# Optimization experiments

Measured on AMD Instinct MI355X. Metric: run time of the kernel, lower is better.

The kernel has to match this reference:

```python
import jax, jax.numpy as jnp
import numpy as np

N_NODES = 4096
N_EDGES = 16384
F_IN = 64
F_EDGE = 16
HID = 128
OUT = 64
N_GRAPHS = 32


def _encoder(x, edge_index, edge_attr, batch, p):
    N = x.shape[0]
    src, dst = edge_index[0], edge_index[1]
    # EdgeMLP: [E, F_edge] -> [E, F_in * HID] per-edge weight matrices
    h = jax.nn.relu(edge_attr @ p['e_w1'] + p['e_b1'])
    h = jax.nn.relu(h @ p['e_w2'] + p['e_b2'])
    Wmat = (h @ p['e_w3'] + p['e_b3']).reshape(-1, x.shape[1], p['root_w'].shape[1])  # [E, F_in, HID]
    # NNConv: message = x_src @ W_edge, scatter-add to dst, plus root transform + bias
    msg = jnp.einsum('ei,eio->eo', x[src], Wmat)  # [E, HID]
    agg = jax.ops.segment_sum(msg, dst, num_segments=N)
    h1 = jax.nn.relu(agg + x @ p['root_w'] + p['conv1_b'])  # [N, HID]
    # GATConv (1 head, concat=False) with self-loops (PyG default)
    loop = jnp.arange(N, dtype=src.dtype)
    si = jnp.concatenate([src, loop])
    di = jnp.concatenate([dst, loop])
    hp = h1 @ p['gat_w']  # [N, HID]
    a_s = hp @ p['att_src']  # [N]
    a_d = hp @ p['att_dst']  # [N]
    e = jax.nn.leaky_relu(a_s[si] + a_d[di], negative_slope=0.2)
    m = jax.ops.segment_max(e, di, num_segments=N)
    ex = jnp.exp(e - m[di])
    denom = jax.ops.segment_sum(ex, di, num_segments=N)
    alpha = ex / (denom[di] + 1e-16)
    h2 = jax.ops.segment_sum(alpha[:, None] * hp[si], di, num_segments=N) + p['gat_b']
    h2 = jax.nn.relu(h2)
    # global mean pool over graphs
    s = jax.ops.segment_sum(h2, batch, num_segments=N_GRAPHS)
    cnt = jax.ops.segment_sum(jnp.ones((N,), h2.dtype), batch, num_segments=N_GRAPHS)
    pooled = s / jnp.maximum(cnt, 1.0)[:, None]
    return jax.nn.relu(pooled @ p['fc1_w'] + p['fc1_b'])  # [B, OUT]


def setup_inputs() -> dict:
    key = jax.random.key(0)
    ks = jax.random.split(key, 24)
    d = {}
    d['x1'] = jax.random.normal(ks[0], (N_NODES, F_IN), jnp.float32)
    d['edge_index1'] = jax.random.randint(ks[1], (2, N_EDGES), 0, N_NODES)
    d['edge_attr1'] = jax.random.normal(ks[2], (N_EDGES, F_EDGE), jnp.float32)
    d['batch1'] = jnp.sort(jax.random.randint(ks[3], (N_NODES,), 0, N_GRAPHS))
    d['x2'] = jax.random.normal(ks[4], (N_NODES, F_IN), jnp.float32)
    d['edge_index2'] = jax.random.randint(ks[5], (2, N_EDGES), 0, N_NODES)
    d['edge_attr2'] = jax.random.normal(ks[6], (N_EDGES, F_EDGE), jnp.float32)
    d['batch2'] = jnp.sort(jax.random.randint(ks[7], (N_NODES,), 0, N_GRAPHS))

    def lin(k, fi, fo):
        return jax.random.normal(k, (fi, fo), jnp.float32) * (fi ** -0.5)

    d['e_w1'] = lin(ks[8], F_EDGE, 128); d['e_b1'] = jnp.zeros((128,), jnp.float32)
    d['e_w2'] = lin(ks[9], 128, 64); d['e_b2'] = jnp.zeros((64,), jnp.float32)
    d['e_w3'] = lin(ks[10], 64, F_IN * HID); d['e_b3'] = jnp.zeros((F_IN * HID,), jnp.float32)
    d['root_w'] = lin(ks[11], F_IN, HID); d['conv1_b'] = jnp.zeros((HID,), jnp.float32)
    d['gat_w'] = lin(ks[12], HID, HID)
    d['att_src'] = jax.random.normal(ks[13], (HID,), jnp.float32) * (HID ** -0.5)
    d['att_dst'] = jax.random.normal(ks[14], (HID,), jnp.float32) * (HID ** -0.5)
    d['gat_b'] = jnp.zeros((HID,), jnp.float32)
    d['fc1_w'] = lin(ks[15], HID, OUT); d['fc1_b'] = jnp.zeros((OUT,), jnp.float32)
    d['fc2_w'] = lin(ks[16], OUT, 1); d['fc2_b'] = jnp.zeros((1,), jnp.float32)
    return d


def reference(x1, edge_index1, edge_attr1, batch1, x2, edge_index2, edge_attr2, batch2,
              e_w1, e_b1, e_w2, e_b2, e_w3, e_b3, root_w, conv1_b,
              gat_w, att_src, att_dst, gat_b, fc1_w, fc1_b, fc2_w, fc2_b):
    p = dict(e_w1=e_w1, e_b1=e_b1, e_w2=e_w2, e_b2=e_b2, e_w3=e_w3, e_b3=e_b3,
             root_w=root_w, conv1_b=conv1_b, gat_w=gat_w, att_src=att_src,
             att_dst=att_dst, gat_b=gat_b, fc1_w=fc1_w, fc1_b=fc1_b,
             fc2_w=fc2_w, fc2_b=fc2_b)
    z1 = _encoder(x1, edge_index1, edge_attr1, batch1, p)
    z2 = _encoder(x2, edge_index2, edge_attr2, batch2, p)
    z = jnp.abs(z1 - z2) @ fc2_w + fc2_b  # [B, 1]
    return jax.nn.sigmoid(z).squeeze(1)  # [B]
```

## Files before the change

### kernel.cpp

```cpp
#include <hip/hip_runtime.h>
#include <hip/hip_bf16.h>
#include <math.h>

#define NN 4096
#define NE 16384
#define FIN 64
#define FE 16
#define HIDD 128
#define OUTD 64
#define NG 32
#define EP (NE + NN)
#define KSPLIT 2
#define NCH (64 / KSPLIT)

typedef __attribute__((ext_vector_type(4))) unsigned u4v;
typedef __attribute__((ext_vector_type(4))) float f4v;
typedef _Float16 f16x8 __attribute__((ext_vector_type(8)));

union FragH { u4v u; f16x8 h; };
union FH2 { _Float16 f[2]; unsigned u; };
union F16x8U { _Float16 f[8]; u4v u; };

#define PB_EMLP  4096
#define PB_BIAS  (PB_EMLP + 4096)
#define PB_HIST  (PB_BIAS + 32)
#define PB_TOTAL (PB_HIST + 64)

__global__ void k_prep(const float* __restrict__ ea0, const float* __restrict__ ea1,
                       const float* __restrict__ w1, const float* __restrict__ b1,
                       const float* __restrict__ w2, const float* __restrict__ b2,
                       const float* __restrict__ w3,
                       const float* __restrict__ X0, const float* __restrict__ X1,
                       const float* __restrict__ b3,
                       const int* __restrict__ ei0, const int* __restrict__ ei1,
                       unsigned short* __restrict__ B1t,
                       float* __restrict__ h0, float* __restrict__ h1g,
                       float* __restrict__ Bb0, float* __restrict__ Bb1,
                       int* __restrict__ rowcnt) {
    int b = blockIdx.x, t = threadIdx.x;
    if (b < PB_EMLP) {
        int gi = b >> 11;
        int e0 = (b & 2047) * 8;
        const float* ea = gi ? ea1 : ea0;
        float* hout = gi ? h1g : h0;
        __shared__ float h1s[8][HIDD];
#pragma unroll
        for (int r = 0; r < 4; ++r) {
            int idx = r * 256 + t;
            int e1 = idx >> 7, j = idx & 127;
            float acc = b1[j];
#pragma unroll
            for (int i = 0; i < FE; ++i) acc += ea[(e0 + e1) * FE + i] * w1[i * HIDD + j];
            h1s[e1][j] = fmaxf(acc, 0.f);
        }
        __syncthreads();
#pragma unroll
        for (int r = 0; r < 2; ++r) {
            int idx = r * 256 + t;
            int e1 = idx >> 6, j = idx & 63;
            float acc = b2[j];
#pragma unroll 16
            for (int k = 0; k < HIDD; ++k) acc += h1s[e1][k] * w2[k * 64 + j];
            hout[(size_t)(e0 + e1) * 64 + j] = fmaxf(acc, 0.f);
        }
    } else if (b < PB_BIAS) {
        int bb = b - PB_EMLP;
        int gi = bb >> 11;
        int n = (bb & 2047) * 2 + (t >> 7);
        int o = t & 127;
        const float* X = gi ? X1 : X0;
        float* Bb = gi ? Bb1 : Bb0;
        float acc = 0.f;
#pragma unroll 16
        for (int i = 0; i < FIN; ++i) acc += X[n * FIN + i] * b3[i * HIDD + o];
        Bb[(size_t)n * HIDD + o] = acc;
    } else if (b < PB_HIST) {
        int tid = (b - PB_BIAS) * 256 + t;
        for (int idx = tid; idx < 2 * EP; idx += 32 * 256) {
            int gi = idx / EP, e = idx % EP;
            const int* dst = (gi ? ei1 : ei0) + NE;
            int d = (e < NE) ? dst[e] : e - NE;
            atomicAdd(&rowcnt[gi * NN + d], 1);
        }
    } else {
        __shared__ float lds[64 * 129];
        int c = b - PB_HIST;
#pragma unroll
        for (int r = 0; r < 32; ++r) {
            int idx = r * 256 + t;
            lds[(idx >> 7) * 129 + (idx & 127)] = w3[(size_t)c * 8192 + idx];
        }
        __syncthreads();
#pragma unroll
        for (int r = 0; r < 32; ++r) {
            int e = r * 256 + t;
            float v = lds[(e & 63) * 129 + (e >> 6)];
            union { _Float16 f; unsigned short u; } cv;
            cv.f = (_Float16)v;
            B1t[(size_t)c * 8192 + e] = cv.u;
        }
    }
}

__global__ void k_scan(const int* __restrict__ rowcnt, int* __restrict__ rowptr,
                       const int* __restrict__ batch0, const int* __restrict__ batch1,
                       int* __restrict__ br) {
    int b = blockIdx.x;
    if (b < 2) {
        int gi = b;
        const int* cnt = rowcnt + gi * NN;
        int* rp = rowptr + gi * (NN + 1);
        int t = threadIdx.x;
        int lane = t & 63, w = t >> 6;
        int base = t * 4;
        int v0 = cnt[base], v1 = cnt[base + 1], v2 = cnt[base + 2], v3 = cnt[base + 3];
        int s = v0 + v1 + v2 + v3;
        int inc = s;
#pragma unroll
        for (int off = 1; off < 64; off <<= 1) {
            int u = __shfl_up(inc, off);
            if (lane >= off) inc += u;
        }
        __shared__ int wsum[16];
        if (lane == 63) wsum[w] = inc;
        __syncthreads();
        if (t < 16) {
            int ws = wsum[t];
            int wi = ws;
#pragma unroll
            for (int off = 1; off < 16; off <<= 1) {
                int u = __shfl_up(wi, off);
                if (t >= off) wi += u;
            }
            wsum[t] = wi - ws;
        }
        __syncthreads();
        int run = wsum[w] + inc - s;
        rp[base] = run; run += v0;
        rp[base + 1] = run; run += v1;
        rp[base + 2] = run; run += v2;
        rp[base + 3] = run; run += v3;
        if (t == 1023) rp[NN] = run;
    } else {
        int t = threadIdx.x;
        if (t < 66) {
            int gi = t / 33, g = t % 33;
            const int* batch = gi ? batch1 : batch0;
            int lo = 0, hi = NN;
            while (lo < hi) {
                int mid = (lo + hi) >> 1;
                if (batch[mid] < g) lo = mid + 1; else hi = mid;
            }
            br[gi * 33 + g] = lo;
        }
    }
}

__global__ void k_fill(const int* __restrict__ ei0, const int* __restrict__ ei1,
                       const int* __restrict__ rowptr, int* __restrict__ cnt2,
                       int* __restrict__ adj) {
    int idx = blockIdx.x * 256 + threadIdx.x;
    if (idx >= 2 * EP) return;
    int gi = idx / EP, e = idx % EP;
    const int* dst = (gi ? ei1 : ei0) + NE;
    int d = (e < NE) ? dst[e] : e - NE;
    int pos = rowptr[gi * (NN + 1) + d] + atomicAdd(&cnt2[gi * NN + d], 1);
    adj[gi * EP + pos] = e;
}

__global__ void __launch_bounds__(128, 2)
k_nnconv(const float* __restrict__ x0, const float* __restrict__ x1,
         const float* __restrict__ h_0, const float* __restrict__ h_1,
         const unsigned short* __restrict__ B1t,
         const float* __restrict__ Bb0, const float* __restrict__ Bb1,
         const int* __restrict__ ei0, const int* __restrict__ ei1,
         _Float16* __restrict__ msgh) {
    __shared__ __align__(16) float sm[32 * 128];
    int gi = blockIdx.z;
    const float* x = gi ? x1 : x0;
    const float* hh = gi ? h_1 : h_0;
    const float* Bb = gi ? Bb1 : Bb0;
    const int* src = gi ? ei1 : ei0;

    int t = threadIdx.x;
    int e0 = blockIdx.x * 64;
    int z = blockIdx.y;
    int ch = t >> 6;
    int l = t & 63, q4 = l >> 4, c16 = l & 15;

    FragH xf[4][2];
    int hb_[4];
#pragma unroll
    for (int mf = 0; mf < 4; ++mf) {
        int s_ = src[e0 + mf * 16 + c16];
        hb_[mf] = (e0 + mf * 16 + c16) * 64 + z * NCH;
        const float* xr = &x[(size_t)s_ * FIN];
#pragma unroll
        for (int kf = 0; kf < 2; ++kf) {
            float xv[8];
            *(float4*)&xv[0] = *(const float4*)&xr[kf * 32 + q4 * 8];
            *(float4*)&xv[4] = *(const float4*)&xr[kf * 32 + q4 * 8 + 4];
            u4v w;
#pragma unroll
            for (int p = 0; p < 4; ++p) {
                FH2 c2;
                c2.f[0] = (_Float16)xv[2 * p];
                c2.f[1] = (_Float16)xv[2 * p + 1];
                w[p] = c2.u;
            }
            xf[mf][kf].u = w;
        }
    }

    f4v acc[4][4];
#pragma unroll
    for (int a = 0; a < 4; ++a)
#pragma unroll
        for (int b = 0; b < 4; ++b) acc[a][b] = (f4v){0.f, 0.f, 0.f, 0.f};

    const u4v* bp = (const u4v*)B1t;

#define LOADF(buf, cg)                                                          \
    {                                                                           \
        const u4v* cp = bp + (size_t)(cg) * 1024;                               \
        _Pragma("unroll") for (int kf = 0; kf < 2; ++kf)                        \
        _Pragma("unroll") for (int nf = 0; nf < 4; ++nf)                        \
            buf[kf * 4 + nf].u = cp[(ch * 64 + nf * 16 + c16) * 8 + kf * 4 + q4]; \
    }

#define DOMFMA(buf)                                                             \
    {                                                                           \
        _Pragma("unroll") for (int mf = 0; mf < 4; ++mf) {                      \
            FH2 hp2;                                                            \
            hp2.f[0] = (_Float16)hvC[mf];                                       \
            hp2.f[1] = hp2.f[0];                                                \
            unsigned hw = hp2.u;                                                \
            FragH hb; hb.u = (u4v){hw, hw, hw, hw};                             \
            _Pragma("unroll") for (int kf = 0; kf < 2; ++kf) {                  \
                FragH a1;                                                       \
                a1.h = hb.h * xf[mf][kf].h;                                     \
                _Pragma("unroll") for (int nf = 0; nf < 4; ++nf)                \
                    acc[mf][nf] = __builtin_amdgcn_mfma_f32_16x16x32_f16(       \
                        a1.h, buf[kf * 4 + nf].h, acc[mf][nf], 0, 0, 0);        \
            }                                                                   \
        }                                                                       \
    }

#define STAGE(buf, cl, DO_H, DO_L)                                              \
    {                                                                           \
        if (DO_H) {                                                             \
            _Pragma("unroll") for (int mf = 0; mf < 4; ++mf)                    \
                hvN[mf] = hh[hb_[mf] + (cl) + 1];                               \
        }                                                                       \
        DOMFMA(buf);                                                            \
        if (DO_L) LOADF(buf, z * NCH + (cl) + 3);                               \
        _Pragma("unroll") for (int mf = 0; mf < 4; ++mf) hvC[mf] = hvN[mf];     \
    }

    FragH bA[8], bB[8], bC[8];
    float hvC[4], hvN[4];
    LOADF(bA, z * NCH + 0);
    LOADF(bB, z * NCH + 1);
    LOADF(bC, z * NCH + 2);
#pragma unroll
    for (int mf = 0; mf < 4; ++mf) hvC[mf] = hh[hb_[mf]];

#pragma unroll 1
    for (int cl = 0; cl < NCH - 5; cl += 3) {
        STAGE(bA, cl, 1, 1);
        STAGE(bB, cl + 1, 1, 1);
        STAGE(bC, cl + 2, 1, 1);
    }
    STAGE(bA, NCH - 5, 1, 1);
    STAGE(bB, NCH - 4, 1, 1);
    STAGE(bC, NCH - 3, 1, 0);
    STAGE(bA, NCH - 2, 1, 0);
    STAGE(bB, NCH - 1, 0, 0);
#undef STAGE
#undef LOADF
#undef DOMFMA

    _Float16* mb = msgh + (size_t)(gi * KSPLIT + z) * NE * HIDD;
    int z0 = (z == 0);
#pragma unroll
    for (int half = 0; half < 2; ++half) {
        if (half) __syncthreads();
#pragma unroll
        for (int mf2 = 0; mf2 < 2; ++mf2) {
            int mf = half * 2 + mf2;
#pragma unroll
            for (int j = 0; j < 4; ++j) {
                int rr = mf2 * 16 + q4 * 4 + j;
#pragma unroll
                for (int nf = 0; nf < 4; ++nf)
                    sm[rr * 128 + ch * 64 + nf * 16 + c16] = acc[mf][nf][j];
            }
        }
        __syncthreads();
#pragma unroll
        for (int it = 0; it < 4; ++it) {
            int u = it * 128 + t;
            int row = u >> 4, c8 = u & 15;
            int eg = e0 + half * 32 + row;
            float v[8];
            *(float4*)&v[0] = *(float4*)&sm[row * 128 + c8 * 8];
            *(float4*)&v[4] = *(float4*)&sm[row * 128 + c8 * 8 + 4];
            if (z0) {
                int s_ = src[eg];
                const float* bbr = &Bb[(size_t)s_ * HIDD + c8 * 8];
#pragma unroll
                for (int j = 0; j < 8; ++j) v[j] += bbr[j];
            }
            F16x8U cv;
#pragma unroll
            for (int j = 0; j < 8; ++j) cv.f[j] = (_Float16)v[j];
            *(u4v*)&mb[(size_t)eg * HIDD + c8 * 8] = cv.u;
        }
    }
}

__global__ void k_h1hp(const _Float16* __restrict__ msgh,
                       const int* __restrict__ rowptr, const int* __restrict__ adj,
                       const float* __restrict__ X0, const float* __restrict__ X1,
                       const float* __restrict__ rw, const float* __restrict__ cb,
                       const float* __restrict__ gw,
                       const float* __restrict__ asw, const float* __restrict__ adw,
                       float* __restrict__ hp0, float* __restrict__ hp1,
                       float* __restrict__ a_s0, float* __restrict__ a_s1,
                       float* __restrict__ a_d0, float* __restrict__ a_d1) {
    int gi = blockIdx.y;
    const float* X = gi ? X1 : X0;
    float* hp = gi ? hp1 : hp0;
    float* a_s = gi ? a_s1 : a_s0;
    float* a_d = gi ? a_d1 : a_d0;
    const int* rp = rowptr + gi * (NN + 1);
    const int* aj = adj + gi * EP;
    const _Float16* m0 = msgh + (size_t)(gi * KSPLIT + 0) * NE * HIDD;
    const _Float16* m1 = msgh + (size_t)(gi * KSPLIT + 1) * NE * HIDD;
    int n0 = blockIdx.x * 16;
    int t = threadIdx.x;
    int o = t & 127, q = t >> 7;
    __shared__ float xsh[16][FIN];
    __shared__ float h1s[16][HIDD];
    __shared__ float s1[16][2], s2[16][2];
#pragma unroll
    for (int r = 0; r < 2; ++r) {
        int idx = r * 512 + t;
        xsh[idx >> 6][idx & 63] = X[(n0 + (idx >> 6)) * FIN + (idx & 63)];
    }
    __syncthreads();
    float accs[4];
#pragma unroll
    for (int nn = 0; nn < 4; ++nn) {
        int n = n0 + q * 4 + nn;
        float acc = cb[o];
        int lo = rp[n], hi = rp[n + 1];
        for (int p = lo; p < hi; ++p) {
            int e = aj[p];
            if (e < NE) {
                size_t eo = (size_t)e * HIDD + o;
                acc += (float)m0[eo] + (float)m1[eo];
            }
        }
        accs[nn] = acc;
    }
#pragma unroll 8
    for (int i = 0; i < FIN; ++i) {
        float w = rw[i * HIDD + o];
#pragma unroll
        for (int nn = 0; nn < 4; ++nn) accs[nn] += xsh[q * 4 + nn][i] * w;
    }
#pragma unroll
    for (int nn = 0; nn < 4; ++nn) h1s[q * 4 + nn][o] = fmaxf(accs[nn], 0.f);
    __syncthreads();
#pragma unroll
    for (int nn = 0; nn < 4; ++nn) accs[nn] = 0.f;
#pragma unroll 8
    for (int k = 0; k < HIDD; ++k) {
        float w = gw[k * HIDD + o];
#pragma unroll
        for (int nn = 0; nn < 4; ++nn) accs[nn] += h1s[q * 4 + nn][k] * w;
    }
#pragma unroll
    for (int nn = 0; nn < 4; ++nn) {
        int n = n0 + q * 4 + nn;
        hp[(size_t)n * HIDD + o] = accs[nn];
        float p1 = accs[nn] * asw[o], p2 = accs[nn] * adw[o];
#pragma unroll
        for (int off = 32; off; off >>= 1) {
            p1 += __shfl_down(p1, off);
            p2 += __shfl_down(p2, off);
        }
        if ((o & 63) == 0) { s1[q * 4 + nn][o >> 6] = p1; s2[q * 4 + nn][o >> 6] = p2; }
    }
    __syncthreads();
    if (t < 16) {
        a_s[n0 + t] = s1[t][0] + s1[t][1];
        a_d[n0 + t] = s2[t][0] + s2[t][1];
    }
}

__global__ void k_gat(const int* __restrict__ rowptr, const int* __restrict__ adj,
                      const int* __restrict__ ei0, const int* __restrict__ ei1,
                      const float* __restrict__ hp0, const float* __restrict__ hp1,
                      const float* __restrict__ as0, const float* __restrict__ as1,
                      const float* __restrict__ ad0, const float* __restrict__ ad1,
                      const float* __restrict__ gb,
                      float* __restrict__ h2_0, float* __restrict__ h2_1) {
    int gi = blockIdx.y;
    const int* src = gi ? ei1 : ei0;
    const float* hp = gi ? hp1 : hp0;
    const float* a_s = gi ? as1 : as0;
    const float* a_d = gi ? ad1 : ad0;
    float* h2 = gi ? h2_1 : h2_0;
    const int* rp = rowptr + gi * (NN + 1);
    const int* aj = adj + gi * EP;
    int w = threadIdx.x >> 6, l = threadIdx.x & 63;
    int n = blockIdx.x * 4 + w;
    int lo = rp[n], deg = rp[n + 1] - lo;
    float adn = a_d[n];
    float m = -1e30f;
    for (int base = 0; base < deg; base += 64) {
        float sc = -1e30f;
        int j = base + l;
        if (j < deg) {
            int e = aj[lo + j];
            int si = (e < NE) ? src[e] : n;
            float xsc = a_s[si] + adn;
            sc = xsc > 0.f ? xsc : 0.2f * xsc;
        }
#pragma unroll
        for (int off = 32; off; off >>= 1) sc = fmaxf(sc, __shfl_xor(sc, off));
        m = fmaxf(m, sc);
    }
    float den = 0.f;
    for (int base = 0; base < deg; base += 64) {
        float ev = 0.f;
        int j = base + l;
        if (j < deg) {
            int e = aj[lo + j];
            int si = (e < NE) ? src[e] : n;
            float xsc = a_s[si] + adn;
            float sc = xsc > 0.f ? xsc : 0.2f * xsc;
            ev = expf(sc - m);
        }
#pragma unroll
        for (int off = 32; off; off >>= 1) ev += __shfl_xor(ev, off);
        den += ev;
    }
    float inv = 1.f / (den + 1e-16f);
    float acc0 = 0.f, acc1 = 0.f;
    for (int j = 0; j < deg; ++j) {
        int e = aj[lo + j];
        int si = (e < NE) ? src[e] : n;
        float xsc = a_s[si] + adn;
        float sc = xsc > 0.f ? xsc : 0.2f * xsc;
        float al = expf(sc - m) * inv;
        acc0 += al * hp[(size_t)si * HIDD + l];
        acc1 += al * hp[(size_t)si * HIDD + 64 + l];
    }
    h2[(size_t)n * HIDD + l] = fmaxf(acc0 + gb[l], 0.f);
    h2[(size_t)n * HIDD + 64 + l] = fmaxf(acc1 + gb[64 + l], 0.f);
}

__global__ void k_poolfc1(const float* __restrict__ h2_0, const float* __restrict__ h2_1,
                          const int* __restrict__ br,
                          const float* __restrict__ w, const float* __restrict__ bias,
                          float* __restrict__ z) {
    int gi = blockIdx.x >> 5, g = blockIdx.x & 31;
    const float* h2 = gi ? h2_1 : h2_0;
    int lo = br[gi * 33 + g], hi = br[gi * 33 + g + 1];
    int t = threadIdx.x;
    __shared__ float pool[HIDD];
    float acc = 0.f;
    for (int n = lo; n < hi; ++n) acc += h2[(size_t)n * HIDD + t];
    pool[t] = acc;
    __syncthreads();
    if (t < 64) {
        float c = fmaxf((float)(hi - lo), 1.f);
        float a = bias[t];
#pragma unroll 16
        for (int o = 0; o < HIDD; ++o) a += (pool[o] / c) * w[o * OUTD + t];
        z[gi * NG * OUTD + g * OUTD + t] = fmaxf(a, 0.f);
    }
}

__global__ void k_final(const float* __restrict__ zz,
                        const float* __restrict__ w, const float* __restrict__ b,
                        float* __restrict__ out) {
    int g = threadIdx.x;
    const float* z1 = zz;
    const float* z2 = zz + NG * OUTD;
    float acc = b[0];
#pragma unroll
    for (int j = 0; j < OUTD; ++j) acc += fabsf(z1[g * OUTD + j] - z2[g * OUTD + j]) * w[j];
    out[g] = 1.f / (1.f + expf(-acc));
}

extern "C" void kernel_launch(void* const* d_in, const int* in_sizes, int n_in,
                              void* d_out, int out_size, void* d_ws, size_t ws_size,
                              hipStream_t stream) {
    const float* x0     = (const float*)d_in[0];
    const int*   ei0    = (const int*)d_in[1];
    const float* ea0    = (const float*)d_in[2];
    const int*   b0     = (const int*)d_in[3];
    const float* x1     = (const float*)d_in[4];
    const int*   ei1    = (const int*)d_in[5];
    const float* ea1    = (const float*)d_in[6];
    const int*   b1     = (const int*)d_in[7];
    const float* e_w1 = (const float*)d_in[8];
    const float* e_b1 = (const float*)d_in[9];
    const float* e_w2 = (const float*)d_in[10];
    const float* e_b2 = (const float*)d_in[11];
    const float* e_w3 = (const float*)d_in[12];
    const float* e_b3 = (const float*)d_in[13];
    const float* root_w = (const float*)d_in[14];
    const float* conv1_b = (const float*)d_in[15];
    const float* gat_w = (const float*)d_in[16];
    const float* att_src = (const float*)d_in[17];
    const float* att_dst = (const float*)d_in[18];
    const float* gat_b = (const float*)d_in[19];
    const float* fc1_w = (const float*)d_in[20];
    const float* fc1_b = (const float*)d_in[21];
    const float* fc2_w = (const float*)d_in[22];
    const float* fc2_b = (const float*)d_in[23];

    float* ws = (float*)d_ws;
    size_t off = 0;
    auto alloc = [&](size_t n) { float* p = ws + off; off += n; return p; };
    int* rowcnt = (int*)alloc(2 * NN);
    int* cnt2   = (int*)alloc(2 * NN);
    size_t zero_elems = off;
    int* rowptr = (int*)alloc(2 * (NN + 1));
    int* br     = (int*)alloc(66);
    int* adj    = (int*)alloc(2 * EP);
    float* h[2]   = {alloc((size_t)NE * 64), alloc((size_t)NE * 64)};
    unsigned short* B1t = (unsigned short*)alloc((size_t)4096 * 128 / 2);
    float* Bb[2]  = {alloc((size_t)NN * HIDD), alloc((size_t)NN * HIDD)};
    _Float16* msgh = (_Float16*)alloc((size_t)2 * KSPLIT * NE * HIDD / 2);
    float* hp[2]  = {alloc((size_t)NN * HIDD), alloc((size_t)NN * HIDD)};
    float* a_s[2] = {alloc(NN), alloc(NN)};
    float* a_d[2] = {alloc(NN), alloc(NN)};
    float* h2[2]  = {alloc((size_t)NN * HIDD), alloc((size_t)NN * HIDD)};
    float* zz     = alloc((size_t)2 * NG * OUTD);

    (void)hipMemsetAsync(ws, 0, zero_elems * 4, stream);
    k_prep<<<PB_TOTAL, 256, 0, stream>>>(ea0, ea1, e_w1, e_b1, e_w2, e_b2, e_w3,
                                         x0, x1, e_b3, ei0, ei1,
                                         B1t, h[0], h[1], Bb[0], Bb[1],
                                         rowcnt);
    k_scan<<<3, 1024, 0, stream>>>(rowcnt, rowptr, b0, b1, br);
    k_fill<<<(2 * EP + 255) / 256, 256, 0, stream>>>(ei0, ei1, rowptr, cnt2, adj);
    k_nnconv<<<dim3(NE / 64, KSPLIT, 2), 128, 0, stream>>>(
        x0, x1, h[0], h[1], B1t, Bb[0], Bb[1], ei0, ei1, msgh);
    k_h1hp<<<dim3(NN / 16, 2), 512, 0, stream>>>(
        msgh, rowptr, adj, x0, x1, root_w, conv1_b, gat_w, att_src, att_dst,
        hp[0], hp[1], a_s[0], a_s[1], a_d[0], a_d[1]);
    k_gat<<<dim3(NN / 4, 2), 256, 0, stream>>>(
        rowptr, adj, ei0, ei1, hp[0], hp[1], a_s[0], a_s[1], a_d[0], a_d[1],
        gat_b, h2[0], h2[1]);
    k_poolfc1<<<64, HIDD, 0, stream>>>(h2[0], h2[1], br, fc1_w, fc1_b, zz);
    k_final<<<1, NG, 0, stream>>>(zz, fc2_w, fc2_b, (float*)d_out);
}
```

Measured before the change: 245.9 us.

## Split NNConv output columns across blocks, store edge hidden in fp16, simplify pipeline

The edge-MLP hidden activations are now stored as fp16 instead of fp32, which halves that intermediate's traffic and lets four chunks be fetched with one vector load. The nnconv grid doubles by splitting the 128 output columns into two 64-column halves per block. This halves the accumulator and B-fragment register footprint, so launch bounds rise to 3 blocks per SIMD. The triple-buffered pipeline becomes a simpler double-buffered loop, which gives up some latency hiding and reloads the gathered x rows in twice as many blocks.

```diff
diff --git a/kernel.cpp b/kernel.cpp
--- a/kernel.cpp
+++ b/kernel.cpp
@@ -34,7 +34,7 @@
                        const float* __restrict__ b3,
                        const int* __restrict__ ei0, const int* __restrict__ ei1,
                        unsigned short* __restrict__ B1t,
-                       float* __restrict__ h0, float* __restrict__ h1g,
+                       _Float16* __restrict__ h0, _Float16* __restrict__ h1g,
                        float* __restrict__ Bb0, float* __restrict__ Bb1,
                        int* __restrict__ rowcnt) {
     int b = blockIdx.x, t = threadIdx.x;
@@ -42,7 +42,7 @@
         int gi = b >> 11;
         int e0 = (b & 2047) * 8;
         const float* ea = gi ? ea1 : ea0;
-        float* hout = gi ? h1g : h0;
+        _Float16* hout = gi ? h1g : h0;
         __shared__ float h1s[8][HIDD];
 #pragma unroll
         for (int r = 0; r < 4; ++r) {
@@ -61,7 +61,7 @@
             float acc = b2[j];
 #pragma unroll 16
             for (int k = 0; k < HIDD; ++k) acc += h1s[e1][k] * w2[k * 64 + j];
-            hout[(size_t)(e0 + e1) * 64 + j] = fmaxf(acc, 0.f);
+            hout[(size_t)(e0 + e1) * 64 + j] = (_Float16)fmaxf(acc, 0.f);
         }
     } else if (b < PB_BIAS) {
         int bb = b - PB_EMLP;
@@ -168,24 +168,25 @@
     adj[gi * EP + pos] = e;
 }
 
-__global__ void __launch_bounds__(128, 2)
+__global__ void __launch_bounds__(128, 3)
 k_nnconv(const float* __restrict__ x0, const float* __restrict__ x1,
-         const float* __restrict__ h_0, const float* __restrict__ h_1,
+         const _Float16* __restrict__ h_0, const _Float16* __restrict__ h_1,
          const unsigned short* __restrict__ B1t,
          const float* __restrict__ Bb0, const float* __restrict__ Bb1,
          const int* __restrict__ ei0, const int* __restrict__ ei1,
          _Float16* __restrict__ msgh) {
-    __shared__ __align__(16) float sm[32 * 128];
+    __shared__ __align__(16) float sm[64 * 68];
     int gi = blockIdx.z;
     const float* x = gi ? x1 : x0;
-    const float* hh = gi ? h_1 : h_0;
+    const _Float16* hh = gi ? h_1 : h_0;
     const float* Bb = gi ? Bb1 : Bb0;
     const int* src = gi ? ei1 : ei0;
 
     int t = threadIdx.x;
     int e0 = blockIdx.x * 64;
-    int z = blockIdx.y;
-    int ch = t >> 6;
+    int cb = blockIdx.y & 1;
+    int z = blockIdx.y >> 1;
+    int wv = t >> 6;
     int l = t & 63, q4 = l >> 4, c16 = l & 15;
 
     FragH xf[4][2];
@@ -212,11 +213,11 @@
         }
     }
 
-    f4v acc[4][4];
+    f4v acc[4][2];
 #pragma unroll
     for (int a = 0; a < 4; ++a)
 #pragma unroll
-        for (int b = 0; b < 4; ++b) acc[a][b] = (f4v){0.f, 0.f, 0.f, 0.f};
+        for (int b = 0; b < 2; ++b) acc[a][b] = (f4v){0.f, 0.f, 0.f, 0.f};
 
     const u4v* bp = (const u4v*)B1t;
 
@@ -224,98 +225,77 @@
     {                                                                           \
         const u4v* cp = bp + (size_t)(cg) * 1024;                               \
         _Pragma("unroll") for (int kf = 0; kf < 2; ++kf)                        \
-        _Pragma("unroll") for (int nf = 0; nf < 4; ++nf)                        \
-            buf[kf * 4 + nf].u = cp[(ch * 64 + nf * 16 + c16) * 8 + kf * 4 + q4]; \
-    }
-
-#define DOMFMA(buf)                                                             \
+        _Pragma("unroll") for (int nf = 0; nf < 2; ++nf)                        \
+            buf[kf * 2 + nf].u =                                                \
+                cp[(cb * 64 + wv * 32 + nf * 16 + c16) * 8 + kf * 4 + q4];      \
+    }
+
+#define DOMFMA(buf, COMP)                                                       \
     {                                                                           \
         _Pragma("unroll") for (int mf = 0; mf < 4; ++mf) {                      \
-            FH2 hp2;                                                            \
-            hp2.f[0] = (_Float16)hvC[mf];                                       \
-            hp2.f[1] = hp2.f[0];                                                \
-            unsigned hw = hp2.u;                                                \
+            unsigned hw = hs[mf].COMP;                                          \
+            hw |= hw << 16;                                                     \
             FragH hb; hb.u = (u4v){hw, hw, hw, hw};                             \
             _Pragma("unroll") for (int kf = 0; kf < 2; ++kf) {                  \
                 FragH a1;                                                       \
                 a1.h = hb.h * xf[mf][kf].h;                                     \
-                _Pragma("unroll") for (int nf = 0; nf < 4; ++nf)                \
+                _Pragma("unroll") for (int nf = 0; nf < 2; ++nf)                \
                     acc[mf][nf] = __builtin_amdgcn_mfma_f32_16x16x32_f16(       \
-                        a1.h, buf[kf * 4 + nf].h, acc[mf][nf], 0, 0, 0);        \
+                        a1.h, buf[kf * 2 + nf].h, acc[mf][nf], 0, 0, 0);        \
             }                                                                   \
         }                                                                       \
     }
 
-#define STAGE(buf, cl, DO_H, DO_L)                                              \
-    {                                                                           \
-        if (DO_H) {                                                             \
-            _Pragma("unroll") for (int mf = 0; mf < 4; ++mf)                    \
-                hvN[mf] = hh[hb_[mf] + (cl) + 1];                               \
-        }                                                                       \
-        DOMFMA(buf);                                                            \
-        if (DO_L) LOADF(buf, z * NCH + (cl) + 3);                               \
-        _Pragma("unroll") for (int mf = 0; mf < 4; ++mf) hvC[mf] = hvN[mf];     \
-    }
-
-    FragH bA[8], bB[8], bC[8];
-    float hvC[4], hvN[4];
-    LOADF(bA, z * NCH + 0);
-    LOADF(bB, z * NCH + 1);
-    LOADF(bC, z * NCH + 2);
-#pragma unroll
-    for (int mf = 0; mf < 4; ++mf) hvC[mf] = hh[hb_[mf]];
-
+    FragH bA[4], bB[4];
+    ushort4 hs[4];
+    LOADF(bA, z * NCH);
 #pragma unroll 1
-    for (int cl = 0; cl < NCH - 5; cl += 3) {
-        STAGE(bA, cl, 1, 1);
-        STAGE(bB, cl + 1, 1, 1);
-        STAGE(bC, cl + 2, 1, 1);
-    }
-    STAGE(bA, NCH - 5, 1, 1);
-    STAGE(bB, NCH - 4, 1, 1);
-    STAGE(bC, NCH - 3, 1, 0);
-    STAGE(bA, NCH - 2, 1, 0);
-    STAGE(bB, NCH - 1, 0, 0);
-#undef STAGE
+    for (int cl = 0; cl < NCH; cl += 4) {
+#pragma unroll
+        for (int mf = 0; mf < 4; ++mf)
+            hs[mf] = *(const ushort4*)&hh[hb_[mf] + cl];
+        LOADF(bB, z * NCH + cl + 1);
+        DOMFMA(bA, x);
+        LOADF(bA, z * NCH + cl + 2);
+        DOMFMA(bB, y);
+        LOADF(bB, z * NCH + cl + 3);
+        DOMFMA(bA, z);
+        if (cl + 4 < NCH) LOADF(bA, z * NCH + cl + 4);
+        DOMFMA(bB, w);
+    }
 #undef LOADF
 #undef DOMFMA
 
     _Float16* mb = msgh + (size_t)(gi * KSPLIT + z) * NE * HIDD;
     int z0 = (z == 0);
 #pragma unroll
-    for (int half = 0; half < 2; ++half) {
-        if (half) __syncthreads();
-#pragma unroll
-        for (int mf2 = 0; mf2 < 2; ++mf2) {
-            int mf = half * 2 + mf2;
-#pragma unroll
-            for (int j = 0; j < 4; ++j) {
-                int rr = mf2 * 16 + q4 * 4 + j;
-#pragma unroll
-                for (int nf = 0; nf < 4; ++nf)
-                    sm[rr * 128 + ch * 64 + nf * 16 + c16] = acc[mf][nf][j];
-            }
-        }
-        __syncthreads();
-#pragma unroll
-        for (int it = 0; it < 4; ++it) {
-            int u = it * 128 + t;
-            int row = u >> 4, c8 = u & 15;
-            int eg = e0 + half * 32 + row;
-            float v[8];
-            *(float4*)&v[0] = *(float4*)&sm[row * 128 + c8 * 8];
-            *(float4*)&v[4] = *(float4*)&sm[row * 128 + c8 * 8 + 4];
-            if (z0) {
-                int s_ = src[eg];
-                const float* bbr = &Bb[(size_t)s_ * HIDD + c8 * 8];
-#pragma unroll
-                for (int j = 0; j < 8; ++j) v[j] += bbr[j];
-            }
-            F16x8U cv;
-#pragma unroll
-            for (int j = 0; j < 8; ++j) cv.f[j] = (_Float16)v[j];
-            *(u4v*)&mb[(size_t)eg * HIDD + c8 * 8] = cv.u;
-        }
+    for (int mf = 0; mf < 4; ++mf)
+#pragma unroll
+        for (int j = 0; j < 4; ++j) {
+            int rr = mf * 16 + q4 * 4 + j;
+            int col = wv * 32 + c16;
+            sm[rr * 68 + col] = acc[mf][0][j];
+            sm[rr * 68 + col + 16] = acc[mf][1][j];
+        }
+    __syncthreads();
+#pragma unroll
+    for (int it = 0; it < 4; ++it) {
+        int u = it * 128 + t;
+        int row = u >> 3, c8 = u & 7;
+        int eg = e0 + row;
+        float v[8];
+        *(float4*)&v[0] = *(float4*)&sm[row * 68 + c8 * 8];
+        *(float4*)&v[4] = *(float4*)&sm[row * 68 + c8 * 8 + 4];
+        if (z0) {
+            int s_ = src[eg];
+            const float* bbr = &Bb[(size_t)s_ * HIDD + cb * 64 + c8 * 8];
+#pragma unroll
+            for (int j = 0; j < 8; ++j) v[j] += bbr[j];
+        }
+        F16x8U cv;
+#pragma unroll
+        for (int j = 0; j < 8; ++j) cv.f[j] = (_Float16)v[j];
+        *(u4v*)&mb[(size_t)eg * HIDD + cb * 64 + c8 * 8] = cv.u;
     }
 }
 
@@ -534,7 +514,8 @@
     int* rowptr = (int*)alloc(2 * (NN + 1));
     int* br     = (int*)alloc(66);
     int* adj    = (int*)alloc(2 * EP);
-    float* h[2]   = {alloc((size_t)NE * 64), alloc((size_t)NE * 64)};
+    _Float16* h[2] = {(_Float16*)alloc((size_t)NE * 64 / 2),
+                      (_Float16*)alloc((size_t)NE * 64 / 2)};
     unsigned short* B1t = (unsigned short*)alloc((size_t)4096 * 128 / 2);
     float* Bb[2]  = {alloc((size_t)NN * HIDD), alloc((size_t)NN * HIDD)};
     _Float16* msgh = (_Float16*)alloc((size_t)2 * KSPLIT * NE * HIDD / 2);
@@ -551,7 +532,7 @@
                                          rowcnt);
     k_scan<<<3, 1024, 0, stream>>>(rowcnt, rowptr, b0, b1, br);
     k_fill<<<(2 * EP + 255) / 256, 256, 0, stream>>>(ei0, ei1, rowptr, cnt2, adj);
-    k_nnconv<<<dim3(NE / 64, KSPLIT, 2), 128, 0, stream>>>(
+    k_nnconv<<<dim3(NE / 64, 2 * KSPLIT, 2), 128, 0, stream>>>(
         x0, x1, h[0], h[1], B1t, Bb[0], Bb[1], ei0, ei1, msgh);
     k_h1hp<<<dim3(NN / 16, 2), 512, 0, stream>>>(
         msgh, rowptr, adj, x0, x1, root_w, conv1_b, gat_w, att_src, att_dst,
```

After: 256.7 us. 1.04x slower.
